# Optimization experiments

Measured on AMD Instinct MI355X. Metric: run time of the kernel, lower is better.

## Reference

```python
import jax, jax.numpy as jnp
import numpy as np

D_MODEL, D_K, D_V = 512, 64, 64
LN_EPS = 1e-6


def setup_inputs() -> dict:
    key = jax.random.key(0)
    ks = jax.random.split(key, 8)
    B, Lq, Lk = 2, 1024, 1024
    q = jax.random.normal(ks[0], (B, Lq, D_MODEL), dtype=jnp.float32)
    k = jax.random.normal(ks[1], (B, Lk, D_MODEL), dtype=jnp.float32)
    v = jax.random.normal(ks[2], (B, Lk, D_MODEL), dtype=jnp.float32)
    s = 1.0 / np.sqrt(D_MODEL)
    Wq = jax.random.normal(ks[3], (D_MODEL, D_K), dtype=jnp.float32) * s
    Wk = jax.random.normal(ks[4], (D_MODEL, D_K), dtype=jnp.float32) * s
    Wv = jax.random.normal(ks[5], (D_MODEL, D_V), dtype=jnp.float32) * s
    v_param = jax.random.normal(ks[6], (D_K,), dtype=jnp.float32)
    Wfc = jax.random.normal(ks[7], (D_V, D_MODEL), dtype=jnp.float32) / np.sqrt(D_V)
    ln_gamma = jnp.ones((D_MODEL,), dtype=jnp.float32)
    ln_beta = jnp.zeros((D_MODEL,), dtype=jnp.float32)
    return {"q": q, "k": k, "v": v, "Wq": Wq, "Wk": Wk, "Wv": Wv,
            "v_param": v_param, "Wfc": Wfc, "ln_gamma": ln_gamma, "ln_beta": ln_beta}


def reference(q, k, v, Wq, Wk, Wv, v_param, Wfc, ln_gamma, ln_beta):
    residual = q
    qp = q @ Wq                      # [B, Lq, d_k]
    kp = k @ Wk                      # [B, Lk, d_k]
    vp = v @ Wv                      # [B, Lk, d_v]
    # additive (Bahdanau) scores: tanh(q_i + k_j) . v_param  -> [B, Lq, Lk]
    scores = jnp.einsum("bqkd,d->bqk", jnp.tanh(qp[:, :, None, :] + kp[:, None, :, :]), v_param)
    attn = jax.nn.softmax(scores, axis=-1)   # dropout is identity in eval mode
    out = jnp.einsum("bqk,bkv->bqv", attn, vp)
    out = out @ Wfc + residual               # [B, Lq, d_model]
    mu = jnp.mean(out, axis=-1, keepdims=True)
    var = jnp.var(out, axis=-1, keepdims=True)
    out = (out - mu) * jax.lax.rsqrt(var + LN_EPS) * ln_gamma + ln_beta
    return out, attn
```

## Files before the change

### kernel.cpp

```cpp
#include <hip/hip_runtime.h>
#include <cstddef>
#include <cstdint>

#define D_MODEL 512
#define DK 64
#define LQ 1024
#define LK 1024
#define NB 2
#define LN_EPS 1e-6f
#define L2E2 2.8853900817779268f

__device__ __forceinline__ uint32_t pack_bf2(float a, float b) {
  uint32_t ua = __float_as_uint(a), ub = __float_as_uint(b);
  ua = (ua + 0x7fffu + ((ua >> 16) & 1u)) >> 16;
  ub = (ub + 0x7fffu + ((ub >> 16) & 1u)) >> 16;
  return (ub << 16) | ua;
}

#define PR_ROWS 16
__global__ __launch_bounds__(256, 4) void proj_kernel(
    const float* __restrict__ q, const float* __restrict__ k,
    const float* __restrict__ v, const float* __restrict__ Wq,
    const float* __restrict__ Wk, const float* __restrict__ Wv,
    const float* __restrict__ v_param, float2* __restrict__ ab_g,
    uint32_t* __restrict__ ekT, float* __restrict__ vp) {
  __shared__ float rows[PR_ROWS][D_MODEL];
  const int tid = threadIdx.x;
  const int type = blockIdx.x >> 7;
  const int r0 = (blockIdx.x & 127) * PR_ROWS;
  const float* __restrict__ in = (type == 0) ? q : (type == 1) ? k : v;
  const float* __restrict__ W = (type == 0) ? Wq : (type == 1) ? Wk : Wv;
  {
    const float4* __restrict__ in4 = (const float4*)(in + (size_t)r0 * D_MODEL);
    float4* r4 = (float4*)&rows[0][0];
#pragma unroll
    for (int t = 0; t < 8; ++t) r4[tid + 256 * t] = in4[tid + 256 * t];
  }
  __syncthreads();
  const int lane = tid & 63;
  const int wv = tid >> 6;
  const int rglob = r0 + wv * 4;
  const float* __restrict__ Wl = W + lane;
  float c0[4] = {0.f, 0.f, 0.f, 0.f}, c1[4] = {0.f, 0.f, 0.f, 0.f};
#pragma unroll 2
  for (int e = 0; e < D_MODEL; e += 4) {
    float w0 = Wl[(size_t)(e + 0) * DK];
    float w1 = Wl[(size_t)(e + 1) * DK];
    float w2 = Wl[(size_t)(e + 2) * DK];
    float w3 = Wl[(size_t)(e + 3) * DK];
#pragma unroll
    for (int r = 0; r < 4; ++r) {
      float4 x = *(const float4*)&rows[wv * 4 + r][e];
      c0[r] = fmaf(x.x, w0, c0[r]);
      c1[r] = fmaf(x.y, w1, c1[r]);
      c0[r] = fmaf(x.z, w2, c0[r]);
      c1[r] = fmaf(x.w, w3, c1[r]);
    }
  }
  float acc[4];
#pragma unroll
  for (int r = 0; r < 4; ++r) acc[r] = c0[r] + c1[r];
  if (type == 0) {
    float vpar = v_param[lane];
#pragma unroll
    for (int r = 0; r < 4; ++r) {
      float iv = __builtin_amdgcn_exp2f(-L2E2 * acc[r]);
      ab_g[(size_t)(rglob + r) * DK + lane] = make_float2(vpar * iv, iv);
    }
  } else if (type == 1) {
    float e4[4], h4[4];
#pragma unroll
    for (int r = 0; r < 4; ++r) {
      e4[r] = __builtin_amdgcn_exp2f(L2E2 * acc[r]);
      h4[r] = __shfl_down(e4[r], 32);
    }
    if (lane < 32) {
      int b = rglob >> 10, j0 = rglob & 1023;
      uint4 pk;
      pk.x = pack_bf2(e4[0], h4[0]);
      pk.y = pack_bf2(e4[1], h4[1]);
      pk.z = pack_bf2(e4[2], h4[2]);
      pk.w = pack_bf2(e4[3], h4[3]);
      *(uint4*)&ekT[(size_t)b * 32 * LK + (size_t)lane * LK + j0] = pk;
    }
  } else {
#pragma unroll
    for (int r = 0; r < 4; ++r) vp[(size_t)(rglob + r) * DK + lane] = acc[r];
  }
}

#define RB 4
__global__ __launch_bounds__(256, 6) void score_kernel(
    const float2* __restrict__ ab_g, const uint32_t* __restrict__ ekT,
    float* __restrict__ attn_out) {
  __shared__ float4 ab4s[RB][32];
  __shared__ float mred[RB][4], sred[RB][4];
  const int tid = threadIdx.x;
  const int row0 = blockIdx.x * RB;
  const int batch = row0 >> 10;
  const uint32_t* __restrict__ ekT_b = ekT + (size_t)batch * 32 * LK;
  {
    int r = tid >> 6, d = tid & 63;
    float2 abv = ab_g[(size_t)(row0 + r) * DK + d];
    ((float2*)&ab4s[r][d & 31])[d >> 5] = abv;
  }
  __syncthreads();

  float acc[RB][4];
#pragma unroll
  for (int r = 0; r < RB; ++r)
#pragma unroll
    for (int jj = 0; jj < 4; ++jj) acc[r][jj] = 0.f;

#pragma unroll 2
  for (int dp = 0; dp < 32; ++dp) {
    float klo[4], khi[4];
#pragma unroll
    for (int jj = 0; jj < 4; ++jj) {
      uint32_t kw = ekT_b[(size_t)dp * LK + tid + jj * 256];
      klo[jj] = __uint_as_float(kw << 16);
      khi[jj] = __uint_as_float(kw & 0xffff0000u);
    }
#pragma unroll
    for (int r = 0; r < RB; ++r) {
      float4 ab = ab4s[r][dp];
#pragma unroll
      for (int jj = 0; jj < 4; ++jj) {
        float x1 = klo[jj] + ab.y, x2 = khi[jj] + ab.w;
        float num = fmaf(ab.z, x1, ab.x * x2);
        acc[r][jj] = fmaf(num, __builtin_amdgcn_rcpf(x1 * x2), acc[r][jj]);
      }
    }
  }

  const int wave = __builtin_amdgcn_readfirstlane(tid >> 6);
  const int lane = tid & 63;

  {
#pragma unroll
    for (int r = 0; r < RB; ++r) {
      float pm = fminf(fminf(acc[r][0], acc[r][1]), fminf(acc[r][2], acc[r][3]));
#pragma unroll
      for (int off = 32; off > 0; off >>= 1) pm = fminf(pm, __shfl_xor(pm, off));
      if (lane == 0) mred[r][wave] = pm;
    }
    __syncthreads();
    float inv[RB];
#pragma unroll
    for (int r = 0; r < RB; ++r) {
      float m = fminf(fminf(mred[r][0], mred[r][1]),
                      fminf(mred[r][2], mred[r][3]));
      float s = 0.f;
#pragma unroll
      for (int jj = 0; jj < 4; ++jj) {
        float e = __builtin_amdgcn_exp2f((m - acc[r][jj]) * L2E2);
        acc[r][jj] = e;
        s += e;
      }
#pragma unroll
      for (int off = 32; off > 0; off >>= 1) s += __shfl_xor(s, off);
      if (lane == 0) sred[r][wave] = s;
    }
    __syncthreads();
#pragma unroll
    for (int r = 0; r < RB; ++r)
      inv[r] = __builtin_amdgcn_rcpf(sred[r][0] + sred[r][1] + sred[r][2] +
                                     sred[r][3]);
#pragma unroll
    for (int r = 0; r < RB; ++r) {
      float* __restrict__ arow = attn_out + (size_t)(row0 + r) * LK;
#pragma unroll
      for (int jj = 0; jj < 4; ++jj)
        arow[tid + jj * 256] = acc[r][jj] * inv[r];
    }
  }
}

__global__ __launch_bounds__(256, 4) void pvfc_kernel(
    const float* __restrict__ attn, const float* __restrict__ vp,
    const float* __restrict__ resid, const float* __restrict__ Wfc,
    const float* __restrict__ gamma, const float* __restrict__ beta,
    float* __restrict__ out) {
  __shared__ float sc[RB][LK];
  __shared__ float4 pvred[4][RB][16];
  __shared__ __align__(16) float ovlT[DK][RB];
  __shared__ float red[2][RB][4];
  const int tid = threadIdx.x;
  const int row0 = blockIdx.x * RB;
  const int batch = row0 >> 10;
  const float* __restrict__ vp_b = vp + (size_t)batch * LK * DK;
  {
    const float4* __restrict__ a4 =
        (const float4*)(attn + (size_t)row0 * LK);
    float4* s4 = (float4*)&sc[0][0];
#pragma unroll
    for (int t = 0; t < 4; ++t) s4[tid + 256 * t] = a4[tid + 256 * t];
  }
  __syncthreads();

  const int wave = __builtin_amdgcn_readfirstlane(tid >> 6);
  const int lane = tid & 63;

  {
    const int jj = lane >> 4, l16 = lane & 15;
    const float4* __restrict__ vp4 = (const float4*)vp_b;
    float4 a[RB];
#pragma unroll
    for (int r = 0; r < RB; ++r) a[r] = make_float4(0.f, 0.f, 0.f, 0.f);
#pragma unroll 4
    for (int it = 0; it < 64; ++it) {
      int j = (wave << 8) + (it << 2) + jj;
      float4 vv = vp4[(size_t)j * (DK / 4) + l16];
#pragma unroll
      for (int r = 0; r < RB; ++r) {
        float pw = sc[r][j];
        a[r].x = fmaf(pw, vv.x, a[r].x);
        a[r].y = fmaf(pw, vv.y, a[r].y);
        a[r].z = fmaf(pw, vv.z, a[r].z);
        a[r].w = fmaf(pw, vv.w, a[r].w);
      }
    }
#pragma unroll
    for (int r = 0; r < RB; ++r) {
      a[r].x += __shfl_xor(a[r].x, 16); a[r].y += __shfl_xor(a[r].y, 16);
      a[r].z += __shfl_xor(a[r].z, 16); a[r].w += __shfl_xor(a[r].w, 16);
      a[r].x += __shfl_xor(a[r].x, 32); a[r].y += __shfl_xor(a[r].y, 32);
      a[r].z += __shfl_xor(a[r].z, 32); a[r].w += __shfl_xor(a[r].w, 32);
    }
    if (jj == 0) {
#pragma unroll
      for (int r = 0; r < RB; ++r) pvred[wave][r][l16] = a[r];
    }
  }
  __syncthreads();
  if (tid < 64) {
    int r = tid >> 4, l16 = tid & 15;
    float4 s = make_float4(0.f, 0.f, 0.f, 0.f);
#pragma unroll
    for (int w = 0; w < 4; ++w) {
      float4 t = pvred[w][r][l16];
      s.x += t.x; s.y += t.y; s.z += t.z; s.w += t.w;
    }
    ovlT[l16 * 4 + 0][r] = s.x;
    ovlT[l16 * 4 + 1][r] = s.y;
    ovlT[l16 * 4 + 2][r] = s.z;
    ovlT[l16 * 4 + 3][r] = s.w;
  }
  __syncthreads();

  {
    const int c0 = tid, c1 = tid + 256;
    float y[RB][2];
#pragma unroll
    for (int r = 0; r < RB; ++r) {
      y[r][0] = resid[(size_t)(row0 + r) * D_MODEL + c0];
      y[r][1] = resid[(size_t)(row0 + r) * D_MODEL + c1];
    }
#pragma unroll 4
    for (int e = 0; e < DK; ++e) {
      float w0 = Wfc[(size_t)e * D_MODEL + c0];
      float w1 = Wfc[(size_t)e * D_MODEL + c1];
      float4 ov = *(const float4*)&ovlT[e][0];
      y[0][0] = fmaf(ov.x, w0, y[0][0]); y[0][1] = fmaf(ov.x, w1, y[0][1]);
      y[1][0] = fmaf(ov.y, w0, y[1][0]); y[1][1] = fmaf(ov.y, w1, y[1][1]);
      y[2][0] = fmaf(ov.z, w0, y[2][0]); y[2][1] = fmaf(ov.z, w1, y[2][1]);
      y[3][0] = fmaf(ov.w, w0, y[3][0]); y[3][1] = fmaf(ov.w, w1, y[3][1]);
    }
#pragma unroll
    for (int r = 0; r < RB; ++r) {
      float s = y[r][0] + y[r][1];
#pragma unroll
      for (int off = 32; off > 0; off >>= 1) s += __shfl_xor(s, off);
      if (lane == 0) red[0][r][wave] = s;
    }
    __syncthreads();
    float mu[RB];
#pragma unroll
    for (int r = 0; r < RB; ++r)
      mu[r] = (red[0][r][0] + red[0][r][1] + red[0][r][2] + red[0][r][3]) *
              (1.0f / D_MODEL);
#pragma unroll
    for (int r = 0; r < RB; ++r) {
      float d0 = y[r][0] - mu[r], d1 = y[r][1] - mu[r];
      float s = d0 * d0 + d1 * d1;
#pragma unroll
      for (int off = 32; off > 0; off >>= 1) s += __shfl_xor(s, off);
      if (lane == 0) red[1][r][wave] = s;
    }
    __syncthreads();
    float g0 = gamma[c0], g1 = gamma[c1], b0 = beta[c0], b1 = beta[c1];
#pragma unroll
    for (int r = 0; r < RB; ++r) {
      float var = (red[1][r][0] + red[1][r][1] + red[1][r][2] + red[1][r][3]) *
                  (1.0f / D_MODEL);
      float rstd = rsqrtf(var + LN_EPS);
      out[(size_t)(row0 + r) * D_MODEL + c0] = (y[r][0] - mu[r]) * rstd * g0 + b0;
      out[(size_t)(row0 + r) * D_MODEL + c1] = (y[r][1] - mu[r]) * rstd * g1 + b1;
    }
  }
}

extern "C" void kernel_launch(void* const* d_in, const int* in_sizes, int n_in,
                              void* d_out, int out_size, void* d_ws,
                              size_t ws_size, hipStream_t stream) {
  const float* q = (const float*)d_in[0];
  const float* k = (const float*)d_in[1];
  const float* v = (const float*)d_in[2];
  const float* Wq = (const float*)d_in[3];
  const float* Wk = (const float*)d_in[4];
  const float* Wv = (const float*)d_in[5];
  const float* v_param = (const float*)d_in[6];
  const float* Wfc = (const float*)d_in[7];
  const float* gamma = (const float*)d_in[8];
  const float* beta = (const float*)d_in[9];

  float* out = (float*)d_out;
  float* attn = out + (size_t)NB * LQ * D_MODEL;

  float* base = (float*)d_ws;
  float2* ab_g = (float2*)base;
  uint32_t* ekT = (uint32_t*)(base + (size_t)2 * NB * LQ * DK);
  float* vp = base + (size_t)2 * NB * LQ * DK + NB * 32 * LK;

  hipLaunchKernelGGL(proj_kernel, dim3(3 * 128), dim3(256), 0, stream, q, k, v,
                     Wq, Wk, Wv, v_param, ab_g, ekT, vp);
  hipLaunchKernelGGL(score_kernel, dim3(NB * LQ / RB), dim3(256), 0, stream,
                     ab_g, ekT, attn);
  hipLaunchKernelGGL(pvfc_kernel, dim3(NB * LQ / RB), dim3(256), 0, stream,
                     attn, vp, q, Wfc, gamma, beta, out);
}
```

Baseline: 63.92 us.

## Fuse score and PV/FC kernels and merge tanh pairs via rational combination

Merges the score/softmax kernel with the PV+FC+LayerNorm kernel, so the attention probabilities are written into shared memory directly instead of being re-read from global memory. The exp(k) table is now stored as fp32 float2 instead of packed bf16, and the per-row q terms are read as float4 straight from global memory instead of being staged in LDS. Two d-pairs are combined into one fraction so each group of four dimensions needs a single reciprocal. This saves rcp instructions and a kernel launch, at the cost of twice the bytes for the k table, more registers, and a risk of overflow in the product of four factors.

```diff
diff --git a/kernel.cpp b/kernel.cpp
--- a/kernel.cpp
+++ b/kernel.cpp
@@ -10,20 +10,13 @@
 #define LN_EPS 1e-6f
 #define L2E2 2.8853900817779268f
 
-__device__ __forceinline__ uint32_t pack_bf2(float a, float b) {
-  uint32_t ua = __float_as_uint(a), ub = __float_as_uint(b);
-  ua = (ua + 0x7fffu + ((ua >> 16) & 1u)) >> 16;
-  ub = (ub + 0x7fffu + ((ub >> 16) & 1u)) >> 16;
-  return (ub << 16) | ua;
-}
-
 #define PR_ROWS 16
 __global__ __launch_bounds__(256, 4) void proj_kernel(
     const float* __restrict__ q, const float* __restrict__ k,
     const float* __restrict__ v, const float* __restrict__ Wq,
     const float* __restrict__ Wk, const float* __restrict__ Wv,
-    const float* __restrict__ v_param, float2* __restrict__ ab_g,
-    uint32_t* __restrict__ ekT, float* __restrict__ vp) {
+    const float* __restrict__ v_param, float4* __restrict__ ab4,
+    float2* __restrict__ ekT2, float* __restrict__ vp) {
   __shared__ float rows[PR_ROWS][D_MODEL];
   const int tid = threadIdx.x;
   const int type = blockIdx.x >> 7;
@@ -42,7 +35,7 @@
   const int rglob = r0 + wv * 4;
   const float* __restrict__ Wl = W + lane;
   float c0[4] = {0.f, 0.f, 0.f, 0.f}, c1[4] = {0.f, 0.f, 0.f, 0.f};
-#pragma unroll 2
+#pragma unroll 4
   for (int e = 0; e < D_MODEL; e += 4) {
     float w0 = Wl[(size_t)(e + 0) * DK];
     float w1 = Wl[(size_t)(e + 1) * DK];
@@ -65,7 +58,11 @@
 #pragma unroll
     for (int r = 0; r < 4; ++r) {
       float iv = __builtin_amdgcn_exp2f(-L2E2 * acc[r]);
-      ab_g[(size_t)(rglob + r) * DK + lane] = make_float2(vpar * iv, iv);
+      float A = vpar * iv, B = iv;
+      float Ah = __shfl_down(A, 32);
+      float Bh = __shfl_down(B, 32);
+      if (lane < 32)
+        ab4[(size_t)(rglob + r) * 32 + lane] = make_float4(A, B, Ah, Bh);
     }
   } else if (type == 1) {
     float e4[4], h4[4];
@@ -76,12 +73,9 @@
     }
     if (lane < 32) {
       int b = rglob >> 10, j0 = rglob & 1023;
-      uint4 pk;
-      pk.x = pack_bf2(e4[0], h4[0]);
-      pk.y = pack_bf2(e4[1], h4[1]);
-      pk.z = pack_bf2(e4[2], h4[2]);
-      pk.w = pack_bf2(e4[3], h4[3]);
-      *(uint4*)&ekT[(size_t)b * 32 * LK + (size_t)lane * LK + j0] = pk;
+      float2* bp = ekT2 + (size_t)b * 32 * LK + (size_t)lane * LK + j0;
+      *(float4*)bp = make_float4(e4[0], h4[0], e4[1], h4[1]);
+      *(float4*)(bp + 2) = make_float4(e4[2], h4[2], e4[3], h4[3]);
     }
   } else {
 #pragma unroll
@@ -90,46 +84,61 @@
 }
 
 #define RB 4
-__global__ __launch_bounds__(256, 6) void score_kernel(
-    const float2* __restrict__ ab_g, const uint32_t* __restrict__ ekT,
+__global__ __launch_bounds__(256, 4) void attn_kernel(
+    const float4* __restrict__ ab4, const float2* __restrict__ ekT2,
+    const float* __restrict__ vp, const float* __restrict__ resid,
+    const float* __restrict__ Wfc, const float* __restrict__ gamma,
+    const float* __restrict__ beta, float* __restrict__ out,
     float* __restrict__ attn_out) {
-  __shared__ float4 ab4s[RB][32];
+  __shared__ float sc[RB][LK];
+  __shared__ float4 pvred[4][RB][16];
+  __shared__ __align__(16) float ovlT[DK][RB];
+  __shared__ float red[2][RB][4];
   __shared__ float mred[RB][4], sred[RB][4];
   const int tid = threadIdx.x;
   const int row0 = blockIdx.x * RB;
   const int batch = row0 >> 10;
-  const uint32_t* __restrict__ ekT_b = ekT + (size_t)batch * 32 * LK;
-  {
-    int r = tid >> 6, d = tid & 63;
-    float2 abv = ab_g[(size_t)(row0 + r) * DK + d];
-    ((float2*)&ab4s[r][d & 31])[d >> 5] = abv;
-  }
-  __syncthreads();
-
-  float acc[RB][4];
-#pragma unroll
-  for (int r = 0; r < RB; ++r)
-#pragma unroll
-    for (int jj = 0; jj < 4; ++jj) acc[r][jj] = 0.f;
-
-#pragma unroll 2
-  for (int dp = 0; dp < 32; ++dp) {
-    float klo[4], khi[4];
+  const float2* __restrict__ ekT_b = ekT2 + (size_t)batch * 32 * LK + tid;
+  const float* __restrict__ vp_b = vp + (size_t)batch * LK * DK;
+  const float4* __restrict__ abr0 = ab4 + (size_t)(row0 + 0) * 32;
+  const float4* __restrict__ abr1 = ab4 + (size_t)(row0 + 1) * 32;
+  const float4* __restrict__ abr2 = ab4 + (size_t)(row0 + 2) * 32;
+  const float4* __restrict__ abr3 = ab4 + (size_t)(row0 + 3) * 32;
+
+  float a0[4] = {0.f, 0.f, 0.f, 0.f};
+  float a1[4] = {0.f, 0.f, 0.f, 0.f};
+  float a2[4] = {0.f, 0.f, 0.f, 0.f};
+  float a3[4] = {0.f, 0.f, 0.f, 0.f};
+
+#pragma unroll
+  for (int qd = 0; qd < 16; ++qd) {
+    float2 k0[4], k1[4];
 #pragma unroll
     for (int jj = 0; jj < 4; ++jj) {
-      uint32_t kw = ekT_b[(size_t)dp * LK + tid + jj * 256];
-      klo[jj] = __uint_as_float(kw << 16);
-      khi[jj] = __uint_as_float(kw & 0xffff0000u);
-    }
-#pragma unroll
-    for (int r = 0; r < RB; ++r) {
-      float4 ab = ab4s[r][dp];
-#pragma unroll
-      for (int jj = 0; jj < 4; ++jj) {
-        float x1 = klo[jj] + ab.y, x2 = khi[jj] + ab.w;
-        float num = fmaf(ab.z, x1, ab.x * x2);
-        acc[r][jj] = fmaf(num, __builtin_amdgcn_rcpf(x1 * x2), acc[r][jj]);
-      }
+      k0[jj] = ekT_b[(size_t)(2 * qd + 0) * LK + jj * 256];
+      k1[jj] = ekT_b[(size_t)(2 * qd + 1) * LK + jj * 256];
+    }
+    float4 P0 = abr0[2 * qd], Q0 = abr0[2 * qd + 1];
+    float4 P1 = abr1[2 * qd], Q1 = abr1[2 * qd + 1];
+    float4 P2 = abr2[2 * qd], Q2 = abr2[2 * qd + 1];
+    float4 P3 = abr3[2 * qd], Q3 = abr3[2 * qd + 1];
+#pragma unroll
+    for (int jj = 0; jj < 4; ++jj) {
+#define QUAD(PP, QQ, ACC)                                                  \
+  {                                                                        \
+    float x1 = k0[jj].x + PP.y, x2 = k0[jj].y + PP.w;                      \
+    float x3 = k1[jj].x + QQ.y, x4 = k1[jj].y + QQ.w;                      \
+    float p12 = x1 * x2, p34 = x3 * x4;                                    \
+    float n12 = fmaf(PP.z, x1, PP.x * x2);                                 \
+    float n34 = fmaf(QQ.z, x3, QQ.x * x4);                                 \
+    float num = fmaf(n34, p12, n12 * p34);                                 \
+    ACC[jj] = fmaf(num, __builtin_amdgcn_rcpf(p12 * p34), ACC[jj]);        \
+  }
+      QUAD(P0, Q0, a0)
+      QUAD(P1, Q1, a1)
+      QUAD(P2, Q2, a2)
+      QUAD(P3, Q3, a3)
+#undef QUAD
     }
   }
 
@@ -137,69 +146,63 @@
   const int lane = tid & 63;
 
   {
-#pragma unroll
-    for (int r = 0; r < RB; ++r) {
-      float pm = fminf(fminf(acc[r][0], acc[r][1]), fminf(acc[r][2], acc[r][3]));
-#pragma unroll
-      for (int off = 32; off > 0; off >>= 1) pm = fminf(pm, __shfl_xor(pm, off));
-      if (lane == 0) mred[r][wave] = pm;
+    float pm0 = fminf(fminf(a0[0], a0[1]), fminf(a0[2], a0[3]));
+    float pm1 = fminf(fminf(a1[0], a1[1]), fminf(a1[2], a1[3]));
+    float pm2 = fminf(fminf(a2[0], a2[1]), fminf(a2[2], a2[3]));
+    float pm3 = fminf(fminf(a3[0], a3[1]), fminf(a3[2], a3[3]));
+#pragma unroll
+    for (int off = 32; off > 0; off >>= 1) {
+      pm0 = fminf(pm0, __shfl_xor(pm0, off));
+      pm1 = fminf(pm1, __shfl_xor(pm1, off));
+      pm2 = fminf(pm2, __shfl_xor(pm2, off));
+      pm3 = fminf(pm3, __shfl_xor(pm3, off));
+    }
+    if (lane == 0) {
+      mred[0][wave] = pm0; mred[1][wave] = pm1;
+      mred[2][wave] = pm2; mred[3][wave] = pm3;
     }
     __syncthreads();
-    float inv[RB];
-#pragma unroll
-    for (int r = 0; r < RB; ++r) {
-      float m = fminf(fminf(mred[r][0], mred[r][1]),
-                      fminf(mred[r][2], mred[r][3]));
-      float s = 0.f;
-#pragma unroll
-      for (int jj = 0; jj < 4; ++jj) {
-        float e = __builtin_amdgcn_exp2f((m - acc[r][jj]) * L2E2);
-        acc[r][jj] = e;
-        s += e;
-      }
-#pragma unroll
-      for (int off = 32; off > 0; off >>= 1) s += __shfl_xor(s, off);
-      if (lane == 0) sred[r][wave] = s;
+    float m0 = fminf(fminf(mred[0][0], mred[0][1]), fminf(mred[0][2], mred[0][3]));
+    float m1 = fminf(fminf(mred[1][0], mred[1][1]), fminf(mred[1][2], mred[1][3]));
+    float m2 = fminf(fminf(mred[2][0], mred[2][1]), fminf(mred[2][2], mred[2][3]));
+    float m3 = fminf(fminf(mred[3][0], mred[3][1]), fminf(mred[3][2], mred[3][3]));
+    float s0 = 0.f, s1 = 0.f, s2 = 0.f, s3 = 0.f;
+#pragma unroll
+    for (int jj = 0; jj < 4; ++jj) {
+      a0[jj] = __builtin_amdgcn_exp2f((m0 - a0[jj]) * L2E2); s0 += a0[jj];
+      a1[jj] = __builtin_amdgcn_exp2f((m1 - a1[jj]) * L2E2); s1 += a1[jj];
+      a2[jj] = __builtin_amdgcn_exp2f((m2 - a2[jj]) * L2E2); s2 += a2[jj];
+      a3[jj] = __builtin_amdgcn_exp2f((m3 - a3[jj]) * L2E2); s3 += a3[jj];
+    }
+#pragma unroll
+    for (int off = 32; off > 0; off >>= 1) {
+      s0 += __shfl_xor(s0, off); s1 += __shfl_xor(s1, off);
+      s2 += __shfl_xor(s2, off); s3 += __shfl_xor(s3, off);
+    }
+    if (lane == 0) {
+      sred[0][wave] = s0; sred[1][wave] = s1;
+      sred[2][wave] = s2; sred[3][wave] = s3;
     }
     __syncthreads();
-#pragma unroll
-    for (int r = 0; r < RB; ++r)
-      inv[r] = __builtin_amdgcn_rcpf(sred[r][0] + sred[r][1] + sred[r][2] +
-                                     sred[r][3]);
-#pragma unroll
-    for (int r = 0; r < RB; ++r) {
-      float* __restrict__ arow = attn_out + (size_t)(row0 + r) * LK;
-#pragma unroll
-      for (int jj = 0; jj < 4; ++jj)
-        arow[tid + jj * 256] = acc[r][jj] * inv[r];
-    }
-  }
-}
-
-__global__ __launch_bounds__(256, 4) void pvfc_kernel(
-    const float* __restrict__ attn, const float* __restrict__ vp,
-    const float* __restrict__ resid, const float* __restrict__ Wfc,
-    const float* __restrict__ gamma, const float* __restrict__ beta,
-    float* __restrict__ out) {
-  __shared__ float sc[RB][LK];
-  __shared__ float4 pvred[4][RB][16];
-  __shared__ __align__(16) float ovlT[DK][RB];
-  __shared__ float red[2][RB][4];
-  const int tid = threadIdx.x;
-  const int row0 = blockIdx.x * RB;
-  const int batch = row0 >> 10;
-  const float* __restrict__ vp_b = vp + (size_t)batch * LK * DK;
-  {
-    const float4* __restrict__ a4 =
-        (const float4*)(attn + (size_t)row0 * LK);
-    float4* s4 = (float4*)&sc[0][0];
-#pragma unroll
-    for (int t = 0; t < 4; ++t) s4[tid + 256 * t] = a4[tid + 256 * t];
+    float i0 = __builtin_amdgcn_rcpf(sred[0][0] + sred[0][1] + sred[0][2] + sred[0][3]);
+    float i1 = __builtin_amdgcn_rcpf(sred[1][0] + sred[1][1] + sred[1][2] + sred[1][3]);
+    float i2 = __builtin_amdgcn_rcpf(sred[2][0] + sred[2][1] + sred[2][2] + sred[2][3]);
+    float i3 = __builtin_amdgcn_rcpf(sred[3][0] + sred[3][1] + sred[3][2] + sred[3][3]);
+    float* __restrict__ ar0 = attn_out + (size_t)(row0 + 0) * LK;
+    float* __restrict__ ar1 = attn_out + (size_t)(row0 + 1) * LK;
+    float* __restrict__ ar2 = attn_out + (size_t)(row0 + 2) * LK;
+    float* __restrict__ ar3 = attn_out + (size_t)(row0 + 3) * LK;
+#pragma unroll
+    for (int jj = 0; jj < 4; ++jj) {
+      float p0 = a0[jj] * i0, p1 = a1[jj] * i1;
+      float p2 = a2[jj] * i2, p3 = a3[jj] * i3;
+      sc[0][tid + jj * 256] = p0; ar0[tid + jj * 256] = p0;
+      sc[1][tid + jj * 256] = p1; ar1[tid + jj * 256] = p1;
+      sc[2][tid + jj * 256] = p2; ar2[tid + jj * 256] = p2;
+      sc[3][tid + jj * 256] = p3; ar3[tid + jj * 256] = p3;
+    }
   }
   __syncthreads();
-
-  const int wave = __builtin_amdgcn_readfirstlane(tid >> 6);
-  const int lane = tid & 63;
 
   {
     const int jj = lane >> 4, l16 = lane & 15;
@@ -318,14 +321,13 @@
   float* attn = out + (size_t)NB * LQ * D_MODEL;
 
   float* base = (float*)d_ws;
-  float2* ab_g = (float2*)base;
-  uint32_t* ekT = (uint32_t*)(base + (size_t)2 * NB * LQ * DK);
-  float* vp = base + (size_t)2 * NB * LQ * DK + NB * 32 * LK;
+  float4* ab4 = (float4*)base;
+  float* p1 = base + (size_t)NB * LQ * 32 * 4;
+  float2* ekT2 = (float2*)p1;
+  float* vp = p1 + (size_t)NB * 32 * LK * 2;
 
   hipLaunchKernelGGL(proj_kernel, dim3(3 * 128), dim3(256), 0, stream, q, k, v,
-                     Wq, Wk, Wv, v_param, ab_g, ekT, vp);
-  hipLaunchKernelGGL(score_kernel, dim3(NB * LQ / RB), dim3(256), 0, stream,
-                     ab_g, ekT, attn);
-  hipLaunchKernelGGL(pvfc_kernel, dim3(NB * LQ / RB), dim3(256), 0, stream,
-                     attn, vp, q, Wfc, gamma, beta, out);
+                     Wq, Wk, Wv, v_param, ab4, ekT2, vp);
+  hipLaunchKernelGGL(attn_kernel, dim3(NB * LQ / RB), dim3(256), 0, stream,
+                     ab4, ekT2, vp, q, Wfc, gamma, beta, out, attn);
 }
```

New measurement: 54.46 us, median of 2. 1.17x faster.
